# Kernel tuning notes

Hardware: AMD Instinct MI355X
Metric: run time of the kernel (lower is better)

## Reference

```python
import jax, jax.numpy as jnp
import numpy as np
from jax import lax

G, BS = 8, 32  # group_num, blocksize


def conv(x, w, b=None, stride=1, pad=0):
    out = lax.conv_general_dilated(x, w, (stride, stride), [(pad, pad), (pad, pad)],
                                   dimension_numbers=('NCHW', 'OIHW', 'NCHW'))
    if b is not None:
        out = out + b[None, :, None, None]
    return out


def prelu(x, a):
    return jnp.where(x >= 0, x, a * x)


def reshape_adap(x, bs):
    # faithful vectorized form of My_Reshape_Adap: channel c = co*bs*bs + p*bs + q
    # goes to output[b, co, i*bs+p, j*bs+q]
    B, C, h, w = x.shape
    co = C // (bs * bs)
    return x.reshape(B, co, bs, bs, h, w).transpose(0, 1, 4, 2, 5, 3).reshape(B, co, h * bs, w * bs)


def setup_inputs() -> dict:
    key = jax.random.key(0)
    ks = jax.random.split(key, 24)
    rn = lambda k, shp, s: (jax.random.normal(k, shp, dtype=jnp.float32) * s)
    inp = {
        'x': rn(ks[0], (1, 1, 256, 256), 1.0),
        'sample_w': rn(ks[1], (G, 13, 1, 32, 32), 0.03),
        'up_w': rn(ks[2], (G, 1024, 13, 1, 1), 0.2),
        'up_b': rn(ks[3], (G, 1024), 0.02),
        'h1_w': rn(ks[4], (G, 64, 1, 3, 3), 0.2),
        'h1_b': rn(ks[5], (G, 64), 0.02),
        'h1_a': jnp.full((G,), 0.25, jnp.float32),
        'fus_w': rn(ks[6], (G - 1, 64, 128, 3, 3), 0.03),
        'fus_b': rn(ks[7], (G - 1, 64), 0.02),
        'fus_a': jnp.full((G - 1,), 0.25, jnp.float32),
        't2_w': rn(ks[8], (G, 64, 64, 3, 3), 0.04),
        't2_b': rn(ks[9], (G, 64), 0.02),
        't2_a': jnp.full((G,), 0.25, jnp.float32),
        't3_w': rn(ks[10], (G, 64, 64, 3, 3), 0.04),
        't3_b': rn(ks[11], (G, 64), 0.02),
        't3_a': jnp.full((G,), 0.25, jnp.float32),
        't4_w': rn(ks[12], (G, 64, 64, 3, 3), 0.04),
        't4_b': rn(ks[13], (G, 64), 0.02),
        't4_a': jnp.full((G,), 0.25, jnp.float32),
        't5_w': rn(ks[14], (G, 1, 64, 3, 3), 0.04),
        't5_b': rn(ks[15], (G, 1), 0.02),
    }
    return inp


def reference(x, sample_w, up_w, up_b, h1_w, h1_b, h1_a, fus_w, fus_b, fus_a,
              t2_w, t2_b, t2_a, t3_w, t3_b, t3_a, t4_w, t4_b, t4_a, t5_w, t5_b):
    outs = []
    feature = None
    for m in range(G):
        # SamplingModule: conv(1->13, k=32, s=32, no bias)
        s = conv(x, sample_w[m], stride=BS)
        # HeadBlock: 1x1 upsample (13->1024) + block scatter reshape + conv(1->64)+PReLU
        u = conv(s, up_w[m], up_b[m])
        r = reshape_adap(u, BS)                       # [B,1,H,W]
        h = prelu(conv(r, h1_w[m], h1_b[m], pad=1), h1_a[m])  # [B,64,H,W]
        if m == 0:
            feature = h
        else:
            # Fusion_concate: conv(128->64)+PReLU on channel concat
            cat = jnp.concatenate([feature, h], axis=1)
            feature = prelu(conv(cat, fus_w[m - 1], fus_b[m - 1], pad=1), fus_a[m - 1])
        t = prelu(conv(feature, t2_w[m], t2_b[m], pad=1), t2_a[m])
        t = prelu(conv(t, t3_w[m], t3_b[m], pad=1), t3_a[m])
        t = prelu(conv(t, t4_w[m], t4_b[m], pad=1), t4_a[m])
        outs.append(conv(t, t5_w[m], t5_b[m], pad=1))
    return jnp.stack(outs)  # [G, B, 1, H, W]
```

## Files before the change

kernel.cpp:

```cpp
#include <hip/hip_runtime.h>

constexpr int H = 256, W = 256, NPIX = H * W;
constexpr int PW = 258;
constexpr size_t PLANE = (size_t)PW * PW * 64;

typedef _Float16 half8 __attribute__((ext_vector_type(8)));
typedef _Float16 half4 __attribute__((ext_vector_type(4)));
typedef float    f32x4 __attribute__((ext_vector_type(4)));
typedef float    f32x16 __attribute__((ext_vector_type(16)));

__device__ __forceinline__ void gl16(const _Float16* g, _Float16* l)
{
    __builtin_amdgcn_global_load_lds(
        (const __attribute__((address_space(1))) unsigned int*)g,
        (__attribute__((address_space(3))) unsigned int*)l, 16, 0, 0);
}

__global__ __launch_bounds__(256)
void prep_k(const float* __restrict__ x, const float* __restrict__ sw,
            const float* __restrict__ uw, const float* __restrict__ ub,
            const float* __restrict__ t2w, const float* __restrict__ t3w,
            const float* __restrict__ t4w, const float* __restrict__ fusw,
            _Float16* __restrict__ planes, _Float16* __restrict__ w16,
            float* __restrict__ r_all)
{
    const int b = blockIdx.x, t = threadIdx.x;
    for (int idx = b * 256 + t; idx < 24 * 1028 * 8; idx += 512 * 256) {
        int c = idx & 7, rem = idx >> 3;
        int p = rem / 1028, bb = rem % 1028;
        int gy, gx;
        if (bb < 258)      { gy = 0;            gx = bb; }
        else if (bb < 516) { gy = 257;          gx = bb - 258; }
        else if (bb < 772) { gy = bb - 516 + 1; gx = 0; }
        else               { gy = bb - 772 + 1; gx = 257; }
        f32x4 z = {0.f, 0.f, 0.f, 0.f};
        *(f32x4*)(planes + (size_t)p * PLANE + ((size_t)(gy * PW + gx) * 64) + c * 8) = z;
    }
    for (int idx = b * 256 + t; idx < 38 * 36864; idx += 512 * 256) {
        int blk = idx / 36864, r2 = idx % 36864;
        int e = r2 & 7, co = (r2 >> 3) & 63, hh = (r2 >> 9) & 1, kk = (r2 >> 10) & 3,
            tap = r2 >> 12;
        const float* src; int cin, cib;
        if (blk < 24) {
            int which = blk >> 3, m = blk & 7;
            src = (which == 0 ? t2w : which == 1 ? t3w : t4w) + (size_t)m * 64 * 64 * 9;
            cin = 64; cib = 0;
        } else {
            int f = (blk - 24) >> 1; cib = ((blk - 24) & 1) * 64;
            src = fusw + (size_t)f * 64 * 128 * 9; cin = 128;
        }
        int ci = cib + (kk * 2 + hh) * 8 + e;
        w16[idx] = (_Float16)src[((size_t)co * cin + ci) * 9 + tap];
    }
    {
        int m = b >> 6, ij = b & 63;
        int i = ij >> 3, j = ij & 7;
        __shared__ float s_lds[16];
        if (t < 208) {
            int c = t >> 4, sub = t & 15;
            float acc = 0.f;
            for (int k = sub * 64; k < sub * 64 + 64; ++k) {
                int p = k >> 5, q = k & 31;
                acc += x[(i * 32 + p) * W + (j * 32 + q)] * sw[(m * 13 + c) * 1024 + k];
            }
            #pragma unroll
            for (int off = 8; off; off >>= 1) acc += __shfl_down(acc, off, 16);
            if (sub == 0) s_lds[c] = acc;
        }
        __syncthreads();
        const float* uwm = uw + m * 1024 * 13;
        float* rm = r_all + m * NPIX;
        #pragma unroll
        for (int pi = 0; pi < 4; ++pi) {
            int px = pi * 256 + t;
            int p = px >> 5, q = px & 31;
            int oc = p * 32 + q;
            float acc = ub[m * 1024 + oc];
            #pragma unroll
            for (int c = 0; c < 13; ++c) acc = fmaf(uwm[oc * 13 + c], s_lds[c], acc);
            rm[((i * 32 + p) << 8) + j * 32 + q] = acc;
        }
    }
}

__global__ __launch_bounds__(256)
void h1_k(const float* __restrict__ r_all, const float* __restrict__ w,
          const float* __restrict__ b, const float* __restrict__ a,
          _Float16* __restrict__ f0)
{
    const float* r = r_all;
    const int t = threadIdx.x;
    const int px = t & 63, cog = t >> 6;
    const int y = blockIdx.x >> 2;
    const int x = ((blockIdx.x & 3) << 6) + px;
    float v[9];
    #pragma unroll
    for (int dy = 0; dy < 3; ++dy) {
        int gy = y + dy - 1;
        #pragma unroll
        for (int dx = 0; dx < 3; ++dx) {
            int gx = x + dx - 1;
            v[dy*3+dx] = ((unsigned)gy < 256u && (unsigned)gx < 256u)
                       ? r[(gy << 8) + gx] : 0.f;
        }
    }
    const float slope = a[0];
    _Float16* op = f0 + ((size_t)((y + 1) * PW + (x + 1))) * 64 + cog * 16;
    #pragma unroll
    for (int cg2 = 0; cg2 < 2; ++cg2) {
        half8 o;
        #pragma unroll
        for (int j = 0; j < 8; ++j) {
            int co = cog * 16 + cg2 * 8 + j;
            float acc = b[co];
            #pragma unroll
            for (int k = 0; k < 9; ++k) acc = fmaf(v[k], w[co*9+k], acc);
            acc = acc >= 0.f ? acc : slope * acc;
            o[j] = (_Float16)acc;
        }
        *(half8*)(op + cg2 * 8) = o;
    }
}

__global__ __launch_bounds__(256, 2)
void conv_mfma_k(const _Float16* __restrict__ in0, const _Float16* __restrict__ w0,
                 const float* __restrict__ bias, const float* __restrict__ alpha,
                 _Float16* __restrict__ out)
{
    const int t    = threadIdx.x;
    const int lane = t & 63;
    const int wv   = t >> 6;
    const int b    = blockIdx.x;
    const int m    = b >> 6;
    const int rem  = b & 63;
    const int xh   = rem & 1;
    const int y0   = (rem >> 1) << 3;

    const _Float16* inp0 = in0 + (size_t)m * PLANE;
    _Float16*       outp = out + (size_t)m * PLANE;
    const _Float16* wp0  = w0 + (size_t)m * 36864;
    const float*    bp   = bias + m * 64;
    const float     slope = alpha[m];
    const int x0 = xh << 7;

    const int h = lane >> 5, cl = lane & 31;
    const int px0 = (wv & 1) * 64, cobase = (wv >> 1) * 32;

    extern __shared__ __align__(16) char smem[];
    _Float16* li = (_Float16*)smem;

    half8 Areg[36];
    #pragma unroll
    for (int tap = 0; tap < 9; ++tap)
        #pragma unroll
        for (int kk = 0; kk < 4; ++kk)
            Areg[tap*4+kk] = *(const half8*)(wp0 +
                (size_t)(((tap*4+kk)*2 + h)*64 + cobase + cl) * 8);

    auto stage_row = [&](int pr) {
        const int slot = pr & 3;
        #pragma unroll
        for (int i = 0; i < 5; ++i) {
            int f = i * 256 + t;
            if (i < 4 || f < 1040) {
                int c = f / 130, hx = f - c * 130;
                gl16(inp0 + ((size_t)(pr * PW + x0 + hx) * 64 + c * 8),
                     li + (size_t)(slot * 1040 + f) * 8);
            }
        }
    };

    f32x16 acc0, acc1;

    stage_row(y0); stage_row(y0 + 1); stage_row(y0 + 2);
    __syncthreads();
    #pragma unroll 1
    for (int s = 0; s < 8; ++s) {
        if (s < 7) stage_row(y0 + s + 3);
        #pragma unroll
        for (int q = 0; q < 4; ++q)
            #pragma unroll
            for (int j = 0; j < 4; ++j) {
                float bb = bp[cobase + q * 8 + 4 * h + j];
                acc0[q*4+j] = bb; acc1[q*4+j] = bb;
            }
        __builtin_amdgcn_s_setprio(1);
        #pragma unroll
        for (int tap = 0; tap < 9; ++tap) {
            const int dy = tap / 3, dx = tap % 3;
            const int slot = (y0 + s + dy) & 3;
            const int hx0 = px0 + cl + dx;
            #pragma unroll
            for (int kk = 0; kk < 4; ++kk) {
                const int c = kk * 2 + h;
                const size_t base = (size_t)(slot * 1040 + c * 130);
                half8 b0 = *(const half8*)(li + (base + hx0) * 8);
                half8 b1 = *(const half8*)(li + (base + hx0 + 32) * 8);
                acc0 = __builtin_amdgcn_mfma_f32_32x32x16_f16(Areg[tap*4+kk], b0, acc0, 0, 0, 0);
                acc1 = __builtin_amdgcn_mfma_f32_32x32x16_f16(Areg[tap*4+kk], b1, acc1, 0, 0, 0);
            }
        }
        __builtin_amdgcn_s_setprio(0);
        const int y = y0 + s;
        #pragma unroll
        for (int pt = 0; pt < 2; ++pt) {
            const size_t gp = (size_t)((y + 1) * PW + (x0 + px0 + pt * 32 + cl + 1)) * 64;
            const f32x16& A0 = pt ? acc1 : acc0;
            #pragma unroll
            for (int q = 0; q < 4; ++q) {
                half4 v0;
                #pragma unroll
                for (int j = 0; j < 4; ++j) {
                    float xv = A0[q*4+j];
                    xv = xv >= 0.f ? xv : slope * xv;
                    v0[j] = (_Float16)xv;
                }
                *(half4*)(outp + gp + cobase + q * 8 + 4 * h) = v0;
            }
        }
        if (s < 7) {
            asm volatile("s_waitcnt vmcnt(8)" ::: "memory");
            __builtin_amdgcn_s_barrier();
            __builtin_amdgcn_sched_barrier(0);
        }
    }
}

__global__ __launch_bounds__(256, 2)
void fus_k(const _Float16* __restrict__ fprev, const float* __restrict__ rm,
           const float* __restrict__ h1w, const float* __restrict__ h1b,
           const float* __restrict__ h1a,
           const _Float16* __restrict__ wf, const _Float16* __restrict__ wh,
           const float* __restrict__ bias, const float* __restrict__ alpha,
           _Float16* __restrict__ outp)
{
    const int t = threadIdx.x, lane = t & 63, wv = t >> 6;
    const int b = blockIdx.x;
    const int xcd = b & 7, u = b >> 3, xq = u & 3, band = u >> 2;
    const int y0 = xcd * 32 + band * 2, x0 = xq * 64;
    const int h = lane >> 5, cl = lane & 31;
    const int px0 = (wv & 1) * 32, cobase = (wv >> 1) * 32;

    __shared__ __align__(16) _Float16 ringF[4 * 528 * 8];
    __shared__ __align__(16) _Float16 ringH[4 * 528 * 8];
    __shared__ float rtile[6 * 68];

    #pragma unroll
    for (int i = 0; i < 9; ++i) {
        int idx = i * 256 + t;
        if (i < 8 || idx < 2112) {
            int r = idx / 528, f = idx - r * 528;
            int hx = f >> 3, c = f & 7;
            gl16(fprev + ((size_t)((y0 + r) * PW + x0 + hx) * 64 + (c ^ (hx & 7)) * 8),
                 ringF + (size_t)idx * 8);
        }
    }

    #pragma unroll
    for (int i = 0; i < 2; ++i) {
        int ix = i * 256 + t;
        if (ix < 408) {
            int row = ix / 68, col = ix - row * 68;
            int gy = y0 - 2 + row, gx = x0 - 2 + col;
            rtile[ix] = ((unsigned)gy < 256u && (unsigned)gx < 256u)
                      ? rm[(gy << 8) + gx] : 0.f;
        }
    }
    asm volatile("s_waitcnt lgkmcnt(0)" ::: "memory");
    __builtin_amdgcn_s_barrier();
    __builtin_amdgcn_sched_barrier(0);

    {
        const int c8 = t & 7;
        float wreg[72];
        #pragma unroll
        for (int i = 0; i < 18; ++i)
            *(f32x4*)(wreg + i * 4) = *(const f32x4*)(h1w + c8 * 72 + i * 4);
        float b8[8];
        #pragma unroll
        for (int j = 0; j < 8; ++j) b8[j] = h1b[c8 * 8 + j];
        const float hs = h1a[0];

        #pragma unroll
        for (int it = 0; it < 9; ++it) {
            int idx = it * 256 + t;
            if (it < 8 || idx < 2112) {
                int pl = idx >> 3;
                int r  = pl / 66, hx = pl - r * 66;
                int gy = y0 - 1 + r, gx = x0 - 1 + hx;
                half8 o = {0,0,0,0,0,0,0,0};
                if ((unsigned)gy < 256u && (unsigned)gx < 256u) {
                    float v[9];
                    #pragma unroll
                    for (int dy = 0; dy < 3; ++dy)
                        #pragma unroll
                        for (int dx = 0; dx < 3; ++dx)
                            v[dy*3+dx] = rtile[(r + dy) * 68 + hx + dx];
                    #pragma unroll
                    for (int j = 0; j < 8; ++j) {
                        float av = b8[j];
                        #pragma unroll
                        for (int k = 0; k < 9; ++k) av = fmaf(v[k], wreg[j*9+k], av);
                        av = av >= 0.f ? av : hs * av;
                        o[j] = (_Float16)av;
                    }
                }
                *(half8*)(ringH + (size_t)(r * 528 + hx * 8 + (c8 ^ (hx & 7))) * 8) = o;
            }
        }
    }
    __builtin_amdgcn_sched_barrier(0);

    half8 Areg[36];
    auto load_A = [&](const _Float16* w) {
        #pragma unroll
        for (int tap = 0; tap < 9; ++tap)
            #pragma unroll
            for (int kk = 0; kk < 4; ++kk)
                Areg[tap*4+kk] = *(const half8*)(w +
                    (size_t)(((tap*4+kk)*2 + h)*64 + cobase + cl) * 8);
    };
    load_A(wf);

    f32x16 acc0, acc1;
    #pragma unroll
    for (int q = 0; q < 4; ++q)
        #pragma unroll
        for (int j = 0; j < 4; ++j) {
            float bb = bias[cobase + q * 8 + 4 * h + j];
            acc0[q*4+j] = bb; acc1[q*4+j] = bb;
        }

    __syncthreads();

    auto cpass = [&](const _Float16* ring) {
        __builtin_amdgcn_s_setprio(1);
        #pragma unroll
        for (int tap = 0; tap < 9; ++tap) {
            const int dy = tap / 3, dx = tap % 3;
            const int hx = px0 + cl + dx;
            const int sw = hx & 7;
            #pragma unroll
            for (int kk = 0; kk < 4; ++kk) {
                const int c = kk * 2 + h;
                half8 b0 = *(const half8*)(ring + ((size_t)(((dy    )*528) + hx*8 + (c ^ sw))) * 8);
                half8 b1 = *(const half8*)(ring + ((size_t)(((dy + 1)*528) + hx*8 + (c ^ sw))) * 8);
                acc0 = __builtin_amdgcn_mfma_f32_32x32x16_f16(Areg[tap*4+kk], b0, acc0, 0, 0, 0);
                acc1 = __builtin_amdgcn_mfma_f32_32x32x16_f16(Areg[tap*4+kk], b1, acc1, 0, 0, 0);
            }
        }
        __builtin_amdgcn_s_setprio(0);
    };

    cpass(ringF);
    load_A(wh);
    cpass(ringH);

    const float slope = alpha[0];
    #pragma unroll
    for (int s = 0; s < 2; ++s) {
        const size_t gp = (size_t)((y0 + s + 1) * PW + (x0 + px0 + cl + 1)) * 64 + cobase;
        const f32x16& A0 = s ? acc1 : acc0;
        #pragma unroll
        for (int q = 0; q < 4; ++q) {
            half4 v;
            #pragma unroll
            for (int j = 0; j < 4; ++j) {
                float xv = A0[q*4+j];
                xv = xv >= 0.f ? xv : slope * xv;
                v[j] = (_Float16)xv;
            }
            *(half4*)(outp + gp + q * 8 + 4 * h) = v;
        }
    }
}

__global__ __launch_bounds__(256, 4)
void t5_k(const _Float16* __restrict__ in_all, const float* __restrict__ w_all,
          const float* __restrict__ b_all, float* __restrict__ out_all)
{
    const int m = blockIdx.y;
    const _Float16* in = in_all + (size_t)m * PLANE;
    const float* w = w_all + m * 576;
    float* outp = out_all + m * NPIX;

    const int t = threadIdx.x;
    const int b = blockIdx.x;
    const int xcd = b & 7, u = b >> 3;
    const int xq = u & 3, band = u >> 2;
    const int y0 = xcd * 32 + band * 8;
    const int x0 = xq << 6;

    __shared__ __align__(16) _Float16 ring[4 * 528 * 8];
    __shared__ float wl[576];
    __shared__ float part[256];

    auto stage_row = [&](int pr) {
        const int slot = pr & 3;
        #pragma unroll
        for (int i = 0; i < 3; ++i) {
            int f = i * 256 + t;
            if (f < 528) {
                int c = f / 66, hx = f - c * 66;
                gl16(in + ((size_t)(pr * PW + x0 + hx) * 64 + c * 8),
                     ring + (size_t)(slot * 528 + f) * 8);
            }
        }
    };

    stage_row(y0); stage_row(y0 + 1); stage_row(y0 + 2);
    #pragma unroll
    for (int i = 0; i < 3; ++i) { int idx = i*256 + t; if (idx < 576) wl[idx] = w[idx]; }
    __syncthreads();

    const int p5 = t & 63, cq = t >> 6;
    #pragma unroll 1
    for (int s = 0; s < 8; ++s) {
        if (s < 7) stage_row(y0 + s + 3);
        float acc = 0.f;
        #pragma unroll
        for (int dy = 0; dy < 3; ++dy) {
            const int slot = (y0 + s + dy) & 3;
            #pragma unroll
            for (int dx = 0; dx < 3; ++dx) {
                const int hx = p5 + dx, tap = dy * 3 + dx;
                #pragma unroll
                for (int c2 = 0; c2 < 2; ++c2) {
                    const int c8 = cq * 2 + c2;
                    half8 vv = *(const half8*)(ring +
                        ((size_t)(slot*528 + c8*66 + hx)) * 8);
                    #pragma unroll
                    for (int e = 0; e < 8; ++e)
                        acc = fmaf((float)vv[e], wl[(c8 * 8 + e) * 9 + tap], acc);
                }
            }
        }
        part[cq * 64 + p5] = acc;
        __syncthreads();
        if (t < 64)
            outp[((y0 + s) << 8) + x0 + t] =
                part[t] + part[64 + t] + part[128 + t] + part[192 + t] + b_all[m];
        __syncthreads();
    }
}

extern "C" void kernel_launch(void* const* d_in, const int* in_sizes, int n_in,
                              void* d_out, int out_size, void* d_ws, size_t ws_size,
                              hipStream_t stream)
{
    const float* x        = (const float*)d_in[0];
    const float* sample_w = (const float*)d_in[1];
    const float* up_w     = (const float*)d_in[2];
    const float* up_b     = (const float*)d_in[3];
    const float* h1_w     = (const float*)d_in[4];
    const float* h1_b     = (const float*)d_in[5];
    const float* h1_a     = (const float*)d_in[6];
    const float* fus_w    = (const float*)d_in[7];
    const float* fus_b    = (const float*)d_in[8];
    const float* fus_a    = (const float*)d_in[9];
    const float* t2_w     = (const float*)d_in[10];
    const float* t2_b     = (const float*)d_in[11];
    const float* t2_a     = (const float*)d_in[12];
    const float* t3_w     = (const float*)d_in[13];
    const float* t3_b     = (const float*)d_in[14];
    const float* t3_a     = (const float*)d_in[15];
    const float* t4_w     = (const float*)d_in[16];
    const float* t4_b     = (const float*)d_in[17];
    const float* t4_a     = (const float*)d_in[18];
    const float* t5_w     = (const float*)d_in[19];
    const float* t5_b     = (const float*)d_in[20];

    float* out = (float*)d_out;
    char*  wsb = (char*)d_ws;

    _Float16* w16    = (_Float16*)wsb;
    float*    r_all  = (float*)(wsb + 2801664);
    _Float16* f_all  = (_Float16*)(wsb + 4898816);
    _Float16* sc_all = f_all + 8 * PLANE;
    _Float16* t1_all = sc_all + 8 * PLANE;

    auto wblk = [&](int b) { return w16 + (size_t)b * 36864; };

    prep_k<<<512, 256, 0, stream>>>(x, sample_w, up_w, up_b,
                                    t2_w, t3_w, t4_w, fus_w,
                                    f_all, w16, r_all);
    h1_k<<<1024, 256, 0, stream>>>(r_all, h1_w, h1_b, h1_a, f_all);

    for (int m = 1; m < 8; ++m) {
        fus_k<<<512, 256, 0, stream>>>(
            f_all + (size_t)(m - 1) * PLANE,
            r_all + m * NPIX, h1_w + m * 576, h1_b + m * 64, h1_a + m,
            wblk(24 + (m - 1) * 2), wblk(24 + (m - 1) * 2 + 1),
            fus_b + (m - 1) * 64, fus_a + (m - 1),
            f_all + (size_t)m * PLANE);
    }

    const size_t LDSB = 66560;
    conv_mfma_k<<<512, 256, LDSB, stream>>>(f_all, wblk(0), t2_b, t2_a, t1_all);
    conv_mfma_k<<<512, 256, LDSB, stream>>>(t1_all, wblk(8), t3_b, t3_a, sc_all);
    conv_mfma_k<<<512, 256, LDSB, stream>>>(sc_all, wblk(16), t4_b, t4_a, t1_all);
    t5_k<<<dim3(128, 8), 256, 0, stream>>>(t1_all, t5_w, t5_b, out);
}
```

Baseline: 343.8 us.

## Store tail-conv intermediates in row-by-channel-group planar layout

The intermediate activation planes written by the tail MFMA convs change from pixel-major layout (64 channels contiguous per pixel) to a layout where each row holds 8 channel groups, each a contiguous run of 8-channel pixels. Row staging into LDS then reads contiguous spans per channel group, and the half4 output stores from each wave land closer together. The conv kernel gets an input-mode flag, the t5 reader and the padding zeroing in prep are changed to match, and only the f_all input keeps the old layout.

```diff
diff --git a/kernel.cpp b/kernel.cpp
--- a/kernel.cpp
+++ b/kernel.cpp
@@ -21,11 +21,11 @@
             const float* __restrict__ uw, const float* __restrict__ ub,
             const float* __restrict__ t2w, const float* __restrict__ t3w,
             const float* __restrict__ t4w, const float* __restrict__ fusw,
-            _Float16* __restrict__ planes, _Float16* __restrict__ w16,
-            float* __restrict__ r_all)
+            _Float16* __restrict__ fplanes, _Float16* __restrict__ cmplanes,
+            _Float16* __restrict__ w16, float* __restrict__ r_all)
 {
     const int b = blockIdx.x, t = threadIdx.x;
-    for (int idx = b * 256 + t; idx < 24 * 1028 * 8; idx += 512 * 256) {
+    for (int idx = b * 256 + t; idx < 8 * 1028 * 8; idx += 512 * 256) {
         int c = idx & 7, rem = idx >> 3;
         int p = rem / 1028, bb = rem % 1028;
         int gy, gx;
@@ -34,7 +34,18 @@
         else if (bb < 772) { gy = bb - 516 + 1; gx = 0; }
         else               { gy = bb - 772 + 1; gx = 257; }
         f32x4 z = {0.f, 0.f, 0.f, 0.f};
-        *(f32x4*)(planes + (size_t)p * PLANE + ((size_t)(gy * PW + gx) * 64) + c * 8) = z;
+        *(f32x4*)(fplanes + (size_t)p * PLANE + ((size_t)(gy * PW + gx) * 64) + c * 8) = z;
+    }
+    for (int idx = b * 256 + t; idx < 16 * 1028 * 8; idx += 512 * 256) {
+        int c = idx & 7, rem = idx >> 3;
+        int p = rem / 1028, bb = rem % 1028;
+        int gy, gx;
+        if (bb < 258)      { gy = 0;            gx = bb; }
+        else if (bb < 516) { gy = 257;          gx = bb - 258; }
+        else if (bb < 772) { gy = bb - 516 + 1; gx = 0; }
+        else               { gy = bb - 772 + 1; gx = 257; }
+        f32x4 z = {0.f, 0.f, 0.f, 0.f};
+        *(f32x4*)(cmplanes + (size_t)p * PLANE + ((size_t)((gy * 8 + c) * PW + gx) * 8)) = z;
     }
     for (int idx = b * 256 + t; idx < 38 * 36864; idx += 512 * 256) {
         int blk = idx / 36864, r2 = idx % 36864;
@@ -125,7 +136,7 @@
 __global__ __launch_bounds__(256, 2)
 void conv_mfma_k(const _Float16* __restrict__ in0, const _Float16* __restrict__ w0,
                  const float* __restrict__ bias, const float* __restrict__ alpha,
-                 _Float16* __restrict__ out)
+                 _Float16* __restrict__ out, int inmode)
 {
     const int t    = threadIdx.x;
     const int lane = t & 63;
@@ -164,8 +175,10 @@
             int f = i * 256 + t;
             if (i < 4 || f < 1040) {
                 int c = f / 130, hx = f - c * 130;
-                gl16(inp0 + ((size_t)(pr * PW + x0 + hx) * 64 + c * 8),
-                     li + (size_t)(slot * 1040 + f) * 8);
+                const _Float16* src = inmode
+                    ? inp0 + ((size_t)((pr * 8 + c) * PW + x0 + hx) * 8)
+                    : inp0 + ((size_t)(pr * PW + x0 + hx) * 64 + c * 8);
+                gl16(src, li + (size_t)(slot * 1040 + f) * 8);
             }
         }
     };
@@ -204,7 +217,7 @@
         const int y = y0 + s;
         #pragma unroll
         for (int pt = 0; pt < 2; ++pt) {
-            const size_t gp = (size_t)((y + 1) * PW + (x0 + px0 + pt * 32 + cl + 1)) * 64;
+            const int gx = x0 + px0 + pt * 32 + cl + 1;
             const f32x16& A0 = pt ? acc1 : acc0;
             #pragma unroll
             for (int q = 0; q < 4; ++q) {
@@ -215,7 +228,8 @@
                     xv = xv >= 0.f ? xv : slope * xv;
                     v0[j] = (_Float16)xv;
                 }
-                *(half4*)(outp + gp + cobase + q * 8 + 4 * h) = v0;
+                const int cq = (cobase >> 3) + q;
+                *(half4*)(outp + ((size_t)(((y + 1) * 8 + cq) * PW + gx) * 8) + 4 * h) = v0;
             }
         }
         if (s < 7) {
@@ -402,7 +416,7 @@
             int f = i * 256 + t;
             if (f < 528) {
                 int c = f / 66, hx = f - c * 66;
-                gl16(in + ((size_t)(pr * PW + x0 + hx) * 64 + c * 8),
+                gl16(in + ((size_t)((pr * 8 + c) * PW + x0 + hx) * 8),
                      ring + (size_t)(slot * 528 + f) * 8);
             }
         }
@@ -483,7 +497,7 @@
 
     prep_k<<<512, 256, 0, stream>>>(x, sample_w, up_w, up_b,
                                     t2_w, t3_w, t4_w, fus_w,
-                                    f_all, w16, r_all);
+                                    f_all, sc_all, w16, r_all);
     h1_k<<<1024, 256, 0, stream>>>(r_all, h1_w, h1_b, h1_a, f_all);
 
     for (int m = 1; m < 8; ++m) {
@@ -496,8 +510,8 @@
     }
 
     const size_t LDSB = 66560;
-    conv_mfma_k<<<512, 256, LDSB, stream>>>(f_all, wblk(0), t2_b, t2_a, t1_all);
-    conv_mfma_k<<<512, 256, LDSB, stream>>>(t1_all, wblk(8), t3_b, t3_a, sc_all);
-    conv_mfma_k<<<512, 256, LDSB, stream>>>(sc_all, wblk(16), t4_b, t4_a, t1_all);
+    conv_mfma_k<<<512, 256, LDSB, stream>>>(f_all, wblk(0), t2_b, t2_a, t1_all, 0);
+    conv_mfma_k<<<512, 256, LDSB, stream>>>(t1_all, wblk(8), t3_b, t3_a, sc_all, 1);
+    conv_mfma_k<<<512, 256, LDSB, stream>>>(sc_all, wblk(16), t4_b, t4_a, t1_all, 1);
     t5_k<<<dim3(128, 8), 256, 0, stream>>>(t1_all, t5_w, t5_b, out);
 }
```

New measurement: 340.4 us. About the same (-1.0%).
